# Optimization experiments

Measured on AMD Instinct MI355X. Metric: run time of the kernel, lower is better.

Reference implementation:

```python
import jax, jax.numpy as jnp
import numpy as np

N_NODES = 100000
N_EDGES = 1000000
D_IN = 64
D_OUT = 64


def setup_inputs() -> dict:
    key = jax.random.key(0)
    k_x, k_e, k_w, k_b = jax.random.split(key, 4)
    x = jax.random.normal(k_x, (N_NODES, D_IN), dtype=jnp.float32)
    edge_index = jax.random.randint(k_e, (2, N_EDGES), 0, N_NODES, dtype=jnp.int64)
    # degrees of destination nodes (what the caller is expected to supply);
    # clamp to >=1 to avoid division by zero for isolated nodes
    deg = jax.ops.segment_sum(jnp.ones((N_EDGES,), jnp.float32), edge_index[1], num_segments=N_NODES)
    node_degrees = jnp.maximum(deg, 1.0)
    W = jax.random.normal(k_w, (D_OUT, D_IN), dtype=jnp.float32) * (1.0 / np.sqrt(D_IN))
    b = jax.random.normal(k_b, (D_OUT,), dtype=jnp.float32) * 0.01
    return {"x": x, "edge_index": edge_index, "node_degrees": node_degrees, "W": W, "b": b}


def reference(x, edge_index, node_degrees, W, b):
    # Original does argsort+cumsum+boundary segment-sum; mathematically this is
    # a scatter-add of gathered neighbor features into dst, i.e. a segment sum.
    src, dst = edge_index[0], edge_index[1]
    agg = jax.ops.segment_sum(x[src], dst, num_segments=x.shape[0])  # [N, D_IN]
    mean = agg / node_degrees[:, None]
    return mean @ W.T + b  # [N, D_OUT]
```

## Files before the change

kernel.cpp:

```cpp
#include <hip/hip_runtime.h>


#define D 64
#define BSHIFT 7
#define BNODES (1 << BSHIFT)
#define CAP 2048
#define GTHREADS 512
#define PERTHREAD (CAP / GTHREADS)
#define MAXB 2048

__device__ inline int detect_stride_block(const unsigned* __restrict__ words,
                                          int E, int* sflag) {
    int t = threadIdx.x;
    if (t < 64) {
        unsigned v = (t < E) ? words[2 * t + 1] : 0u;
        int any = __any(v != 0u);
        if (t == 0) *sflag = any ? 1 : 2;
    }
    __syncthreads();
    return *sflag;
}

__device__ inline unsigned pack_bf16(float a, float b) {
    unsigned ua = __float_as_uint(a), ub = __float_as_uint(b);
    ua += 0x7fffu + ((ua >> 16) & 1u);
    ub += 0x7fffu + ((ub >> 16) & 1u);
    return (ua >> 16) | (ub & 0xffff0000u);
}

__global__ __launch_bounds__(256, 4) void partition_xw_kernel(
        const unsigned* __restrict__ ewords, int* __restrict__ cursor,
        unsigned* __restrict__ pairs, uint2* __restrict__ spill,
        int* __restrict__ spillCnt,
        const float* __restrict__ x, const float* __restrict__ W,
        unsigned* __restrict__ y2, int E, int N, int nb, int pblocks) {
    __shared__ __align__(16) char smem[34832];
    int t = threadIdx.x;

    if ((int)blockIdx.x < pblocks) {
        int* lhist = (int*)smem;
        int* lbase = lhist + MAXB;
        int* sflag = lbase + MAXB;
        int s = detect_stride_block(ewords, E, sflag);
        for (int sub = 0; sub < 2; ++sub) {
            int base = blockIdx.x * 8192 + sub * 4096;
            if (base >= E) break;
            for (int i = t; i < nb; i += 256) lhist[i] = 0;
            __syncthreads();
            unsigned pv[16]; int bk[16];
            #pragma unroll
            for (int k = 0; k < 16; ++k) {
                int e = base + k * 256 + t;
                bk[k] = -1;
                if (e < E) {
                    unsigned src = ewords[(size_t)e * s];
                    unsigned dst = ewords[((size_t)E + e) * s];
                    bk[k] = (int)(dst >> BSHIFT);
                    pv[k] = src | ((dst & (BNODES - 1)) << 17);
                    atomicAdd(&lhist[bk[k]], 1);
                }
            }
            __syncthreads();
            for (int hb = t; hb < nb; hb += 256) {
                int cc = lhist[hb];
                if (cc) lbase[hb] = atomicAdd(&cursor[hb], cc);
                lhist[hb] = 0;
            }
            __syncthreads();
            #pragma unroll
            for (int k = 0; k < 16; ++k) {
                if (bk[k] >= 0) {
                    int lpos = lbase[bk[k]] + atomicAdd(&lhist[bk[k]], 1);
                    if (lpos < CAP) {
                        pairs[(size_t)bk[k] * CAP + lpos] = pv[k];
                    } else {
                        int si = atomicAdd(spillCnt, 1);
                        unsigned dst = ((unsigned)bk[k] << BSHIFT) | (pv[k] >> 17);
                        spill[si] = make_uint2(pv[k] & 0x1FFFFu, dst);
                    }
                }
            }
            __syncthreads();
        }
    } else {
        float* Wt = (float*)smem;
        float* xs = Wt + 64 * 68;
        for (int i = t; i < 64 * 64; i += 256) {
            int o = i >> 6, k = i & 63;
            Wt[k * 68 + o] = W[i];
        }
        int base = ((int)blockIdx.x - pblocks) * 64;
        int row = t >> 4, c4 = (t & 15) * 4;
        #pragma unroll
        for (int r = 0; r < 4; ++r) {
            int nl = row + r * 16;
            int n = base + nl;
            float4 v = {0.f, 0.f, 0.f, 0.f};
            if (n < N) v = *(const float4*)(x + (size_t)n * 64 + c4);
            *(float4*)&xs[nl * 68 + c4] = v;
        }
        __syncthreads();
        int o4 = (t & 15) * 4, nl4 = (t >> 4) * 4;
        float acc[4][4];
        #pragma unroll
        for (int i = 0; i < 4; ++i)
            #pragma unroll
            for (int j = 0; j < 4; ++j) acc[i][j] = 0.f;
        #pragma unroll 2
        for (int k0 = 0; k0 < 64; k0 += 4) {
            float a[4][4], wv[4][4];
            #pragma unroll
            for (int i = 0; i < 4; ++i)
                *(float4*)a[i] = *(const float4*)&xs[(nl4 + i) * 68 + k0];
            #pragma unroll
            for (int dk = 0; dk < 4; ++dk)
                *(float4*)wv[dk] = *(const float4*)&Wt[(k0 + dk) * 68 + o4];
            #pragma unroll
            for (int i = 0; i < 4; ++i)
                #pragma unroll
                for (int j = 0; j < 4; ++j)
                    acc[i][j] += a[i][0] * wv[0][j] + a[i][1] * wv[1][j]
                               + a[i][2] * wv[2][j] + a[i][3] * wv[3][j];
        }
        int n0 = base + nl4;
        #pragma unroll
        for (int i = 0; i < 4; ++i) {
            if (n0 + i < N) {
                uint2 p;
                p.x = pack_bf16(acc[i][0], acc[i][1]);
                p.y = pack_bf16(acc[i][2], acc[i][3]);
                *(uint2*)(y2 + (size_t)(n0 + i) * 32 + (o4 >> 1)) = p;
            }
        }
    }
}

__global__ __launch_bounds__(GTHREADS) void bucket_gather(
        const unsigned* __restrict__ y2, const unsigned* __restrict__ pairs,
        const int* __restrict__ cursor, const uint2* __restrict__ spill,
        const int* __restrict__ spillCnt,
        const float* __restrict__ deg, const float* __restrict__ b,
        float* __restrict__ out, int N) {
    __shared__ unsigned list[CAP];
    __shared__ int cnt[BNODES], st[BNODES], sc[BNODES];
    int t = threadIdx.x;
    int bkt = blockIdx.x, base = bkt << BSHIFT;
    int total = cursor[bkt];
    int cn = total < CAP ? total : CAP;
    int lane = t & 63, w = t >> 6;
    int g = lane >> 4, c = lane & 15;
    float4 bv = ((const float4*)b)[c];

    if (t < BNODES) cnt[t] = 0;
    __syncthreads();
    unsigned pv[PERTHREAD];
    #pragma unroll
    for (int j = 0; j < PERTHREAD; ++j) {
        int i = t + j * GTHREADS;
        pv[j] = (i < cn) ? pairs[(size_t)bkt * CAP + i] : 0xFFFFFFFFu;
        if (i < cn) atomicAdd(&cnt[pv[j] >> 17], 1);
    }
    __syncthreads();
    if (t < BNODES) sc[t] = cnt[t];
    __syncthreads();
    for (int off = 1; off < BNODES; off <<= 1) {
        int v = (t < BNODES && t >= off) ? sc[t - off] : 0;
        __syncthreads();
        if (t < BNODES) sc[t] += v;
        __syncthreads();
    }
    if (t < BNODES) { st[t] = sc[t] - cnt[t]; sc[t] = sc[t] - cnt[t]; }
    __syncthreads();
    #pragma unroll
    for (int j = 0; j < PERTHREAD; ++j) {
        if (pv[j] != 0xFFFFFFFFu) {
            int pos = atomicAdd(&sc[pv[j] >> 17], 1);
            list[pos] = pv[j] & 0x1FFFFu;
        }
    }
    __syncthreads();

    int scnt = *spillCnt;

    for (int nl0 = w * 16; nl0 < w * 16 + 16; nl0 += 4) {
        int mynode = nl0 + g;
        int n = base + mynode;
        int s0 = st[mynode], e1 = s0 + cnt[mynode];
        float ax = 0.f, ay = 0.f, az = 0.f, aw = 0.f;
        for (int i = s0; i < e1; ++i) {
            unsigned src = list[i];
            uint2 u = *(const uint2*)(y2 + (size_t)src * 32 + c * 2);
            ax += __uint_as_float(u.x << 16);
            ay += __uint_as_float(u.x & 0xffff0000u);
            az += __uint_as_float(u.y << 16);
            aw += __uint_as_float(u.y & 0xffff0000u);
        }
        for (int i = 0; i < scnt; ++i) {
            uint2 e = spill[i];
            if ((int)e.y == n) {
                uint2 u = *(const uint2*)(y2 + (size_t)e.x * 32 + c * 2);
                ax += __uint_as_float(u.x << 16);
                ay += __uint_as_float(u.x & 0xffff0000u);
                az += __uint_as_float(u.y << 16);
                aw += __uint_as_float(u.y & 0xffff0000u);
            }
        }
        if (n < N) {
            float invd = 1.0f / deg[n];
            float4 o4 = {ax * invd + bv.x, ay * invd + bv.y,
                         az * invd + bv.z, aw * invd + bv.w};
            *(float4*)(out + (size_t)n * 64 + c * 4) = o4;
        }
    }
}

__global__ __launch_bounds__(256) void scatter_kernel(
        const float* __restrict__ x, const unsigned* __restrict__ ewords,
        float* __restrict__ agg, int E) {
    __shared__ int sflag;
    int s = detect_stride_block(ewords, E, &sflag);
    int gid = blockIdx.x * blockDim.x + threadIdx.x;
    int e = gid >> 4, q = gid & 15;
    if (e >= E) return;
    int src = (int)ewords[(size_t)e * s];
    int dst = (int)ewords[((size_t)E + e) * s];
    const float4 v = *(const float4*)(x + (size_t)src * D + q * 4);
    float* p = agg + (size_t)dst * D + q * 4;
    unsafeAtomicAdd(p + 0, v.x);
    unsafeAtomicAdd(p + 1, v.y);
    unsafeAtomicAdd(p + 2, v.z);
    unsafeAtomicAdd(p + 3, v.w);
}

__global__ __launch_bounds__(256) void gemm_kernel(
        float* __restrict__ inout, const float* __restrict__ deg,
        const float* __restrict__ W, const float* __restrict__ b, int nNodes) {
    __shared__ float Wt[64 * 65];
    __shared__ float rows[4 * 64];
    int t = threadIdx.x;
    for (int i = t; i < 64 * 64; i += 256) {
        int o = i >> 6, k = i & 63;
        Wt[k * 65 + o] = W[i];
    }
    int base = blockIdx.x * 4;
    int nl = t >> 6, o = t & 63;
    int n = base + nl;
    if (n < nNodes) {
        float invd = 1.0f / deg[n];
        rows[nl * 64 + o] = inout[(size_t)n * 64 + o] * invd;
    }
    __syncthreads();
    if (n >= nNodes) return;
    float acc = b[o];
    #pragma unroll
    for (int k = 0; k < 64; ++k)
        acc += rows[nl * 64 + k] * Wt[k * 65 + o];
    inout[(size_t)n * 64 + o] = acc;
}

extern "C" void kernel_launch(void* const* d_in, const int* in_sizes, int n_in,
                              void* d_out, int out_size, void* d_ws, size_t ws_size,
                              hipStream_t stream) {
    const float*    x      = (const float*)d_in[0];
    const unsigned* ewords = (const unsigned*)d_in[1];
    const float*    deg    = (const float*)d_in[2];
    const float*    W      = (const float*)d_in[3];
    const float*    b      = (const float*)d_in[4];
    float*          out    = (float*)d_out;

    const int E = in_sizes[1] / 2;
    const int N = in_sizes[2];
    const int nb = (N + BNODES - 1) >> BSHIFT;

    char* ws = (char*)d_ws;
    size_t curB  = (MAXB + 16) * 4;
    size_t pairB = ((size_t)nb * CAP * 4 + 63) & ~63ull;
    size_t spB   = ((size_t)E * 8 + 63) & ~63ull;
    size_t need  = curB + pairB + spB + (size_t)N * 32 * 4;

    if (ws_size >= need && N < (1 << 17) && nb <= MAXB) {
        int*      cursor   = (int*)ws;
        int*      spillCnt = cursor + MAXB;
        unsigned* pairs    = (unsigned*)(ws + curB);
        uint2*    spill    = (uint2*)(ws + curB + pairB);
        unsigned* y2       = (unsigned*)(ws + curB + pairB + spB);

        hipMemsetAsync(cursor, 0, curB, stream);

        int pblocks  = (E + 8191) / 8192;
        int xwblocks = (N + 63) / 64;
        partition_xw_kernel<<<pblocks + xwblocks, 256, 0, stream>>>(
            ewords, cursor, pairs, spill, spillCnt, x, W, y2, E, N, nb, pblocks);

        bucket_gather<<<nb, GTHREADS, 0, stream>>>(
            y2, pairs, cursor, spill, spillCnt, deg, b, out, N);
    } else {
        hipMemsetAsync(d_out, 0, (size_t)out_size * sizeof(float), stream);
        long long sthreads = (long long)E * 16;
        int sblocks = (int)((sthreads + 255) / 256);
        scatter_kernel<<<sblocks, 256, 0, stream>>>(x, ewords, out, E);
        gemm_kernel<<<(N + 3) / 4, 256, 0, stream>>>(out, deg, W, b, N);
    }
}
```

Baseline: 147.5 us.

## Widen partition/xw blocks to 512 threads and unroll gather by two

Raises the partition/xw kernel to 512 threads per block. Each partition block now handles 8192 edges in a single pass, dropping the two-pass sub-loop, and each xw block computes 128 nodes instead of 64, with shared memory enlarged to fit. The bucket gather inner loop is unrolled by two with separate accumulators, so two independent neighbor loads are in flight at once. The larger blocks and shared memory may reduce occupancy, and fewer, larger blocks change load balance.

After: 140.8 us. 4.5% less time.

```diff
diff --git a/kernel.cpp b/kernel.cpp
--- a/kernel.cpp
+++ b/kernel.cpp
@@ -7,6 +7,7 @@
 #define CAP 2048
 #define GTHREADS 512
 #define PERTHREAD (CAP / GTHREADS)
+#define PXW_THREADS 512
 #define MAXB 2048
 
 __device__ inline int detect_stride_block(const unsigned* __restrict__ words,
@@ -28,13 +29,13 @@
     return (ua >> 16) | (ub & 0xffff0000u);
 }
 
-__global__ __launch_bounds__(256, 4) void partition_xw_kernel(
+__global__ __launch_bounds__(PXW_THREADS, 4) void partition_xw_kernel(
         const unsigned* __restrict__ ewords, int* __restrict__ cursor,
         unsigned* __restrict__ pairs, uint2* __restrict__ spill,
         int* __restrict__ spillCnt,
         const float* __restrict__ x, const float* __restrict__ W,
         unsigned* __restrict__ y2, int E, int N, int nb, int pblocks) {
-    __shared__ __align__(16) char smem[34832];
+    __shared__ __align__(16) char smem[52240];
     int t = threadIdx.x;
 
     if ((int)blockIdx.x < pblocks) {
@@ -42,58 +43,54 @@
         int* lbase = lhist + MAXB;
         int* sflag = lbase + MAXB;
         int s = detect_stride_block(ewords, E, sflag);
-        for (int sub = 0; sub < 2; ++sub) {
-            int base = blockIdx.x * 8192 + sub * 4096;
-            if (base >= E) break;
-            for (int i = t; i < nb; i += 256) lhist[i] = 0;
-            __syncthreads();
-            unsigned pv[16]; int bk[16];
-            #pragma unroll
-            for (int k = 0; k < 16; ++k) {
-                int e = base + k * 256 + t;
-                bk[k] = -1;
-                if (e < E) {
-                    unsigned src = ewords[(size_t)e * s];
-                    unsigned dst = ewords[((size_t)E + e) * s];
-                    bk[k] = (int)(dst >> BSHIFT);
-                    pv[k] = src | ((dst & (BNODES - 1)) << 17);
-                    atomicAdd(&lhist[bk[k]], 1);
+        int base = blockIdx.x * 8192;
+        for (int i = t; i < nb; i += PXW_THREADS) lhist[i] = 0;
+        __syncthreads();
+        unsigned pv[16]; int bk[16];
+        #pragma unroll
+        for (int k = 0; k < 16; ++k) {
+            int e = base + k * PXW_THREADS + t;
+            bk[k] = -1;
+            if (e < E) {
+                unsigned src = ewords[(size_t)e * s];
+                unsigned dst = ewords[((size_t)E + e) * s];
+                bk[k] = (int)(dst >> BSHIFT);
+                pv[k] = src | ((dst & (BNODES - 1)) << 17);
+                atomicAdd(&lhist[bk[k]], 1);
+            }
+        }
+        __syncthreads();
+        for (int hb = t; hb < nb; hb += PXW_THREADS) {
+            int cc = lhist[hb];
+            if (cc) lbase[hb] = atomicAdd(&cursor[hb], cc);
+            lhist[hb] = 0;
+        }
+        __syncthreads();
+        #pragma unroll
+        for (int k = 0; k < 16; ++k) {
+            if (bk[k] >= 0) {
+                int lpos = lbase[bk[k]] + atomicAdd(&lhist[bk[k]], 1);
+                if (lpos < CAP) {
+                    pairs[(size_t)bk[k] * CAP + lpos] = pv[k];
+                } else {
+                    int si = atomicAdd(spillCnt, 1);
+                    unsigned dst = ((unsigned)bk[k] << BSHIFT) | (pv[k] >> 17);
+                    spill[si] = make_uint2(pv[k] & 0x1FFFFu, dst);
                 }
             }
-            __syncthreads();
-            for (int hb = t; hb < nb; hb += 256) {
-                int cc = lhist[hb];
-                if (cc) lbase[hb] = atomicAdd(&cursor[hb], cc);
-                lhist[hb] = 0;
-            }
-            __syncthreads();
-            #pragma unroll
-            for (int k = 0; k < 16; ++k) {
-                if (bk[k] >= 0) {
-                    int lpos = lbase[bk[k]] + atomicAdd(&lhist[bk[k]], 1);
-                    if (lpos < CAP) {
-                        pairs[(size_t)bk[k] * CAP + lpos] = pv[k];
-                    } else {
-                        int si = atomicAdd(spillCnt, 1);
-                        unsigned dst = ((unsigned)bk[k] << BSHIFT) | (pv[k] >> 17);
-                        spill[si] = make_uint2(pv[k] & 0x1FFFFu, dst);
-                    }
-                }
-            }
-            __syncthreads();
         }
     } else {
         float* Wt = (float*)smem;
         float* xs = Wt + 64 * 68;
-        for (int i = t; i < 64 * 64; i += 256) {
+        for (int i = t; i < 64 * 64; i += PXW_THREADS) {
             int o = i >> 6, k = i & 63;
             Wt[k * 68 + o] = W[i];
         }
-        int base = ((int)blockIdx.x - pblocks) * 64;
+        int base = ((int)blockIdx.x - pblocks) * 128;
         int row = t >> 4, c4 = (t & 15) * 4;
         #pragma unroll
         for (int r = 0; r < 4; ++r) {
-            int nl = row + r * 16;
+            int nl = row + r * 32;
             int n = base + nl;
             float4 v = {0.f, 0.f, 0.f, 0.f};
             if (n < N) v = *(const float4*)(x + (size_t)n * 64 + c4);
@@ -187,16 +184,32 @@
         int n = base + mynode;
         int s0 = st[mynode], e1 = s0 + cnt[mynode];
         float ax = 0.f, ay = 0.f, az = 0.f, aw = 0.f;
-        for (int i = s0; i < e1; ++i) {
-            unsigned src = list[i];
-            uint2 u = *(const uint2*)(y2 + (size_t)src * 32 + c * 2);
+        float bx = 0.f, by = 0.f, bz = 0.f, bw = 0.f;
+        int i = s0;
+        for (; i + 1 < e1; i += 2) {
+            unsigned s0v = list[i], s1v = list[i + 1];
+            uint2 u0 = *(const uint2*)(y2 + (size_t)s0v * 32 + c * 2);
+            uint2 u1 = *(const uint2*)(y2 + (size_t)s1v * 32 + c * 2);
+            ax += __uint_as_float(u0.x << 16);
+            ay += __uint_as_float(u0.x & 0xffff0000u);
+            az += __uint_as_float(u0.y << 16);
+            aw += __uint_as_float(u0.y & 0xffff0000u);
+            bx += __uint_as_float(u1.x << 16);
+            by += __uint_as_float(u1.x & 0xffff0000u);
+            bz += __uint_as_float(u1.y << 16);
+            bw += __uint_as_float(u1.y & 0xffff0000u);
+        }
+        if (i < e1) {
+            unsigned sv = list[i];
+            uint2 u = *(const uint2*)(y2 + (size_t)sv * 32 + c * 2);
             ax += __uint_as_float(u.x << 16);
             ay += __uint_as_float(u.x & 0xffff0000u);
             az += __uint_as_float(u.y << 16);
             aw += __uint_as_float(u.y & 0xffff0000u);
         }
-        for (int i = 0; i < scnt; ++i) {
-            uint2 e = spill[i];
+        ax += bx; ay += by; az += bz; aw += bw;
+        for (int k = 0; k < scnt; ++k) {
+            uint2 e = spill[k];
             if ((int)e.y == n) {
                 uint2 u = *(const uint2*)(y2 + (size_t)e.x * 32 + c * 2);
                 ax += __uint_as_float(u.x << 16);
@@ -288,8 +301,8 @@
         hipMemsetAsync(cursor, 0, curB, stream);
 
         int pblocks  = (E + 8191) / 8192;
-        int xwblocks = (N + 63) / 64;
-        partition_xw_kernel<<<pblocks + xwblocks, 256, 0, stream>>>(
+        int xwblocks = (N + 127) / 128;
+        partition_xw_kernel<<<pblocks + xwblocks, PXW_THREADS, 0, stream>>>(
             ewords, cursor, pairs, spill, spillCnt, x, W, y2, E, N, nb, pblocks);
 
         bucket_gather<<<nb, GTHREADS, 0, stream>>>(
```
